# Optimization experiments

Measured on AMD Instinct MI355X. Metric: run time of the kernel, lower is better.

Reference implementation:

```python
import jax, jax.numpy as jnp
import numpy as np

N, K, D, E = 30000, 20, 128, 600000


def time_encode(t, w, b):
    # TGN TimeEncode: cos(Linear(1->D)(t)) ; t: [...], returns [..., D]
    return jnp.cos(t[..., None] * w + b)


def setup_inputs() -> dict:
    key = jax.random.key(0)
    ks = jax.random.split(key, 8)
    node_features = jax.random.normal(ks[0], (N, D), dtype=jnp.float32)
    timestamps = jax.random.uniform(ks[1], (N,), dtype=jnp.float32) * 1e4
    edge_features = jax.random.normal(ks[2], (E, D), dtype=jnp.float32)
    neighbors = jax.random.randint(ks[3], (N, K), 0, N, dtype=jnp.int32)
    edge_idxs = jax.random.randint(ks[4], (N, K), 0, E, dtype=jnp.int32)
    # edge interaction times precede the query timestamps (temporal neighbor sampling)
    edge_times = jax.random.uniform(ks[5], (N, K), dtype=jnp.float32) * timestamps[:, None]
    # TGN basis-frequency init for the time encoder
    time_w = (1.0 / 10.0 ** np.linspace(0, 9, D)).astype(np.float32)
    time_w = jnp.asarray(time_w)
    time_b = jnp.zeros((D,), dtype=jnp.float32)
    s1 = 1.0 / np.sqrt(3 * D)
    W1 = jax.random.normal(ks[6], (3 * D, D), dtype=jnp.float32) * s1
    b1 = jnp.zeros((D,), dtype=jnp.float32)
    W2 = jax.random.normal(ks[7], (3 * D, D), dtype=jnp.float32) * s1
    b2 = jnp.zeros((D,), dtype=jnp.float32)
    return {"node_features": node_features, "timestamps": timestamps,
            "edge_features": edge_features, "neighbors": neighbors,
            "edge_idxs": edge_idxs, "edge_times": edge_times,
            "time_w": time_w, "time_b": time_b,
            "W1": W1, "b1": b1, "W2": W2, "b2": b2}


def reference(node_features, timestamps, edge_features, neighbors, edge_idxs,
              edge_times, time_w, time_b, W1, b1, W2, b2):
    # layer-0 neighbor embeddings = raw node features gathered at neighbor ids
    neigh_feat = node_features[neighbors]                       # [N, K, D]
    # time deltas between query time and edge times, then cosine time encoding
    deltas = timestamps[:, None] - edge_times                   # [N, K]
    edge_time_emb = time_encode(deltas, time_w, time_b)         # [N, K, D]
    edge_feat = edge_features[edge_idxs]                        # [N, K, D]
    # GraphSumEmbedding.aggregate
    neighbors_features = jnp.concatenate(
        [neigh_feat, edge_time_emb, edge_feat], axis=-1)        # [N, K, 3D]
    h = neighbors_features @ W1 + b1                            # [N, K, D]
    neighbors_sum = jax.nn.relu(jnp.sum(h, axis=1))             # [N, D]
    src_time_emb = time_encode(jnp.zeros_like(timestamps), time_w, time_b)  # [N, D]
    source_features = jnp.concatenate([node_features, src_time_emb], axis=1)
    source_embedding = jnp.concatenate([neighbors_sum, source_features], axis=1)
    return source_embedding @ W2 + b2                           # [N, D]
```

## Files before the change

### kernel.cpp

```cpp
#include <hip/hip_runtime.h>
#include <math.h>

#define DD 128
#define KNB 20
#define K3 384
#define NPB 8

typedef unsigned short u16;
typedef __attribute__((ext_vector_type(8))) short short8;
typedef __attribute__((ext_vector_type(4))) float f32x4;

static __device__ __forceinline__ u16 f2bf(float x) {
    union { float f; unsigned u; } v; v.f = x;
    unsigned r = v.u + 0x7fffu + ((v.u >> 16) & 1u);
    return (u16)(r >> 16);
}

static __device__ __forceinline__ float fcos(float x) {
    float r = x * 0.15915494309189535f;
    r = __builtin_amdgcn_fractf(r);
    return __builtin_amdgcn_cosf(r);
}

static __device__ __forceinline__ void st4bf(u16* p, float4 v) {
    ushort4 s;
    s.x = f2bf(v.x); s.y = f2bf(v.y); s.z = f2bf(v.z); s.w = f2bf(v.w);
    *(ushort4*)p = s;
}

__global__ __launch_bounds__(DD) void const_kernel(
    const float* __restrict__ tb, const float* __restrict__ W2,
    const float* __restrict__ b2, float* __restrict__ cvec)
{
    int d = threadIdx.x;
    float acc = b2[d];
    #pragma unroll 8
    for (int i = 0; i < DD; ++i)
        acc = fmaf(cosf(tb[i]), W2[(size_t)(2 * DD + i) * DD + d], acc);
    cvec[d] = acc;
}

__global__ __launch_bounds__(256) void pack_w(
    const float* __restrict__ W1, const float* __restrict__ W2,
    u16* __restrict__ W1p, u16* __restrict__ W2p)
{
    int t = blockIdx.x * 256 + threadIdx.x;
    if (t < 6144) {
        int L = t & 63;
        int ct = (t >> 6) & 7;
        int kt = t >> 9;
        int n  = ct * 16 + (L & 15);
        int kb = kt * 32 + (L >> 4) * 8;
        u16* d = W1p + (size_t)t * 8;
        #pragma unroll
        for (int j = 0; j < 8; ++j) d[j] = f2bf(W1[(size_t)(kb + j) * DD + n]);
    } else if (t < 10240) {
        int u = t - 6144;
        int L = u & 63;
        int ct = (u >> 6) & 7;
        int kt = (u >> 9) & 3;
        int part = u >> 11;
        int n  = ct * 16 + (L & 15);
        int kb = part * DD + kt * 32 + (L >> 4) * 8;
        u16* d = W2p + (size_t)u * 8;
        #pragma unroll
        for (int j = 0; j < 8; ++j) d[j] = f2bf(W2[(size_t)(kb + j) * DD + n]);
    }
}

__global__ __launch_bounds__(256) void agg_kernel(
    const float* __restrict__ nodef, const float* __restrict__ ts,
    const float* __restrict__ edgef, const int* __restrict__ neighbors,
    const int* __restrict__ edge_idxs, const float* __restrict__ edge_times,
    const float* __restrict__ tw, const float* __restrict__ tb,
    u16* __restrict__ aggbf, u16* __restrict__ nfbf, int N)
{
    __shared__ int   s_nb[NPB * KNB];
    __shared__ int   s_eg[NPB * KNB];
    __shared__ float s_dt[NPB * KNB];

    const int tid = threadIdx.x;
    const int n0  = blockIdx.x * NPB;

    if (tid < NPB * KNB) {
        int nsub = tid / KNB;
        int k    = tid - nsub * KNB;
        int nn   = n0 + nsub;
        if (nn < N) {
            s_nb[tid] = neighbors[(size_t)nn * KNB + k];
            s_eg[tid] = edge_idxs[(size_t)nn * KNB + k];
            s_dt[tid] = ts[nn] - edge_times[(size_t)nn * KNB + k];
        } else {
            s_nb[tid] = 0; s_eg[tid] = 0; s_dt[tid] = 0.f;
        }
    }
    __syncthreads();

    const int c    = tid & 31;
    const int nsub = tid >> 5;
    const int n    = n0 + nsub;

    const float4* nf4 = (const float4*)nodef;
    const float4* ef4 = (const float4*)edgef;
    const float4  w4  = ((const float4*)tw)[c];
    const float4  b4  = ((const float4*)tb)[c];

    float4 an = make_float4(0.f, 0.f, 0.f, 0.f);
    float4 ae = an, at = an;

    const int*   nb  = s_nb + nsub * KNB;
    const int*   eg  = s_eg + nsub * KNB;
    const float* dtp = s_dt + nsub * KNB;

    #pragma unroll 10
    for (int k = 0; k < KNB; ++k) {
        int   ni = nb[k];
        int   ei = eg[k];
        float dt = dtp[k];
        float4 nv = nf4[(size_t)ni * 32 + c];
        float4 ev = ef4[(size_t)ei * 32 + c];
        an.x += nv.x; an.y += nv.y; an.z += nv.z; an.w += nv.w;
        ae.x += ev.x; ae.y += ev.y; ae.z += ev.z; ae.w += ev.w;
        at.x += fcos(fmaf(dt, w4.x, b4.x));
        at.y += fcos(fmaf(dt, w4.y, b4.y));
        at.z += fcos(fmaf(dt, w4.z, b4.z));
        at.w += fcos(fmaf(dt, w4.w, b4.w));
    }

    if (n < N) {
        u16* o = aggbf + (size_t)n * K3;
        st4bf(o + 4 * c,           an);
        st4bf(o + DD + 4 * c,      at);
        st4bf(o + 2 * DD + 4 * c,  ae);
        float4 sf = nf4[(size_t)n * 32 + c];
        st4bf(nfbf + (size_t)n * DD + 4 * c, sf);
    }
}

#define APITCH 392
#define HPITCH 136

__global__ __launch_bounds__(256) void fused_gemm(
    const u16* __restrict__ aggbf, const u16* __restrict__ nfbf,
    const u16* __restrict__ W1p, const u16* __restrict__ W2p,
    const float* __restrict__ b1, const float* __restrict__ cvec,
    float* __restrict__ out, int N)
{
    __shared__ __align__(16) u16 As[32 * APITCH];

    const int tid  = threadIdx.x;
    const int lane = tid & 63;
    const int wave = tid >> 6;
    const int row0 = blockIdx.x * 32;
    const int m0     = (wave & 1) * 16;
    const int ctbase = (wave >> 1) * 4;
    const int l15  = lane & 15;
    const int quad = lane >> 4;

    {
        const float4* ag4 = (const float4*)aggbf;
        #pragma unroll
        for (int i = 0; i < 6; ++i) {
            int idx = tid + i * 256;
            int r = idx / 48, c = idx - r * 48;
            float4 v = make_float4(0.f, 0.f, 0.f, 0.f);
            int row = row0 + r;
            if (row < N) v = ag4[(size_t)row * 48 + c];
            *(float4*)&As[r * APITCH + c * 8] = v;
        }
    }
    __syncthreads();

    f32x4 acc[4];
    #pragma unroll
    for (int c = 0; c < 4; ++c) acc[c] = (f32x4){0.f, 0.f, 0.f, 0.f};

    const short8* W1v = (const short8*)W1p;
    for (int kt = 0; kt < 12; ++kt) {
        short8 a = *(const short8*)&As[(m0 + l15) * APITCH + kt * 32 + quad * 8];
        #pragma unroll
        for (int c = 0; c < 4; ++c) {
            short8 b = W1v[(size_t)(kt * 8 + ctbase + c) * 64 + lane];
            acc[c] = __builtin_amdgcn_mfma_f32_16x16x32_bf16(a, b, acc[c], 0, 0, 0);
        }
    }
    __syncthreads();

    u16* Hs  = As;
    u16* NFs = As + 32 * HPITCH;
    #pragma unroll
    for (int c = 0; c < 4; ++c) {
        int col = (ctbase + c) * 16 + l15;
        float bb = (float)KNB * b1[col];
        #pragma unroll
        for (int r = 0; r < 4; ++r) {
            float h = acc[c][r] + bb;
            h = h > 0.f ? h : 0.f;
            Hs[(m0 + quad * 4 + r) * HPITCH + col] = f2bf(h);
        }
    }
    {
        const float4* nf4 = (const float4*)nfbf;
        #pragma unroll
        for (int i = 0; i < 2; ++i) {
            int idx = tid + i * 256;
            int r = idx >> 4, c = idx & 15;
            float4 v = make_float4(0.f, 0.f, 0.f, 0.f);
            int row = row0 + r;
            if (row < N) v = nf4[(size_t)row * 16 + c];
            *(float4*)&NFs[r * HPITCH + c * 8] = v;
        }
    }
    __syncthreads();

    f32x4 acc2[4];
    #pragma unroll
    for (int c = 0; c < 4; ++c) {
        float cv = cvec[(ctbase + c) * 16 + l15];
        acc2[c] = (f32x4){cv, cv, cv, cv};
    }
    const short8* W2v = (const short8*)W2p;
    for (int kt = 0; kt < 4; ++kt) {
        short8 aH = *(const short8*)&Hs[(m0 + l15) * HPITCH + kt * 32 + quad * 8];
        #pragma unroll
        for (int c = 0; c < 4; ++c) {
            short8 b = W2v[(size_t)(kt * 8 + ctbase + c) * 64 + lane];
            acc2[c] = __builtin_amdgcn_mfma_f32_16x16x32_bf16(aH, b, acc2[c], 0, 0, 0);
        }
        short8 aN = *(const short8*)&NFs[(m0 + l15) * HPITCH + kt * 32 + quad * 8];
        #pragma unroll
        for (int c = 0; c < 4; ++c) {
            short8 b = W2v[(size_t)((4 + kt) * 8 + ctbase + c) * 64 + lane];
            acc2[c] = __builtin_amdgcn_mfma_f32_16x16x32_bf16(aN, b, acc2[c], 0, 0, 0);
        }
    }

    #pragma unroll
    for (int c = 0; c < 4; ++c) {
        int col = (ctbase + c) * 16 + l15;
        #pragma unroll
        for (int r = 0; r < 4; ++r) {
            int row = row0 + m0 + quad * 4 + r;
            if (row < N) out[(size_t)row * DD + col] = acc2[c][r];
        }
    }
}

extern "C" void kernel_launch(void* const* d_in, const int* in_sizes, int n_in,
                              void* d_out, int out_size, void* d_ws, size_t ws_size,
                              hipStream_t stream)
{
    const float* nodef      = (const float*)d_in[0];
    const float* ts         = (const float*)d_in[1];
    const float* edgef      = (const float*)d_in[2];
    const int*   neighbors  = (const int*)d_in[3];
    const int*   edge_idxs  = (const int*)d_in[4];
    const float* edge_times = (const float*)d_in[5];
    const float* tw         = (const float*)d_in[6];
    const float* tb         = (const float*)d_in[7];
    const float* W1         = (const float*)d_in[8];
    const float* b1         = (const float*)d_in[9];
    const float* W2         = (const float*)d_in[10];
    const float* b2         = (const float*)d_in[11];
    float*       out        = (float*)d_out;

    const int N = in_sizes[1];

    u16*   aggbf = (u16*)d_ws;
    u16*   nfbf  = aggbf + (size_t)N * K3;
    u16*   W1p   = nfbf + (size_t)N * DD;
    u16*   W2p   = W1p + 12 * 8 * 64 * 8;
    float* cvec  = (float*)(W2p + 2 * 4 * 8 * 64 * 8);

    hipLaunchKernelGGL(const_kernel, dim3(1), dim3(DD), 0, stream,
                       tb, W2, b2, cvec);
    hipLaunchKernelGGL(pack_w, dim3(40), dim3(256), 0, stream,
                       W1, W2, W1p, W2p);
    hipLaunchKernelGGL(agg_kernel, dim3((N + NPB - 1) / NPB), dim3(256), 0, stream,
                       nodef, ts, edgef, neighbors, edge_idxs, edge_times,
                       tw, tb, aggbf, nfbf, N);
    hipLaunchKernelGGL(fused_gemm, dim3((N + 31) / 32), dim3(256), 0, stream,
                       aggbf, nfbf, W1p, W2p, b1, cvec, out, N);
}
```

Before: 481.2 us.

## Fuse neighbor aggregation with both GEMMs and merge the prep kernels

Merges the aggregation kernel and the two-stage MFMA GEMM into one kernel that keeps the aggregated bf16 rows and node features in LDS. This removes the global round trip through the aggbf/nfbf workspace. Each block now handles 16 rows, with each thread-group gathering two rows, and the four waves split the output columns. The weight-packing and constant-vector kernels are also combined into a single launch. The trade-off is a smaller M tile per block, so each block reloads the weight fragments over fewer rows.

```diff
diff --git a/kernel.cpp b/kernel.cpp
--- a/kernel.cpp
+++ b/kernel.cpp
@@ -4,7 +4,7 @@
 #define DD 128
 #define KNB 20
 #define K3 384
-#define NPB 8
+#define ROWS 16
 
 typedef unsigned short u16;
 typedef __attribute__((ext_vector_type(8))) short short8;
@@ -28,220 +28,211 @@
     *(ushort4*)p = s;
 }
 
-__global__ __launch_bounds__(DD) void const_kernel(
-    const float* __restrict__ tb, const float* __restrict__ W2,
-    const float* __restrict__ b2, float* __restrict__ cvec)
+__global__ __launch_bounds__(256) void prep_kernel(
+    const float* __restrict__ W1, const float* __restrict__ W2,
+    const float* __restrict__ tb, const float* __restrict__ b2,
+    u16* __restrict__ W1p, u16* __restrict__ W2p, float* __restrict__ cvec)
 {
-    int d = threadIdx.x;
-    float acc = b2[d];
-    #pragma unroll 8
-    for (int i = 0; i < DD; ++i)
-        acc = fmaf(cosf(tb[i]), W2[(size_t)(2 * DD + i) * DD + d], acc);
-    cvec[d] = acc;
-}
-
-__global__ __launch_bounds__(256) void pack_w(
-    const float* __restrict__ W1, const float* __restrict__ W2,
-    u16* __restrict__ W1p, u16* __restrict__ W2p)
-{
-    int t = blockIdx.x * 256 + threadIdx.x;
-    if (t < 6144) {
-        int L = t & 63;
-        int ct = (t >> 6) & 7;
-        int kt = t >> 9;
-        int n  = ct * 16 + (L & 15);
-        int kb = kt * 32 + (L >> 4) * 8;
-        u16* d = W1p + (size_t)t * 8;
-        #pragma unroll
-        for (int j = 0; j < 8; ++j) d[j] = f2bf(W1[(size_t)(kb + j) * DD + n]);
-    } else if (t < 10240) {
-        int u = t - 6144;
-        int L = u & 63;
-        int ct = (u >> 6) & 7;
-        int kt = (u >> 9) & 3;
-        int part = u >> 11;
-        int n  = ct * 16 + (L & 15);
-        int kb = part * DD + kt * 32 + (L >> 4) * 8;
-        u16* d = W2p + (size_t)u * 8;
-        #pragma unroll
-        for (int j = 0; j < 8; ++j) d[j] = f2bf(W2[(size_t)(kb + j) * DD + n]);
-    }
-}
-
-__global__ __launch_bounds__(256) void agg_kernel(
+    const int tid = threadIdx.x;
+    if (blockIdx.x < 40) {
+        int t = blockIdx.x * 256 + tid;
+        if (t < 6144) {
+            int L = t & 63;
+            int ct = (t >> 6) & 7;
+            int kt = t >> 9;
+            int n  = ct * 16 + (L & 15);
+            int kb = kt * 32 + (L >> 4) * 8;
+            u16* d = W1p + (size_t)t * 8;
+            #pragma unroll
+            for (int j = 0; j < 8; ++j) d[j] = f2bf(W1[(size_t)(kb + j) * DD + n]);
+        } else if (t < 10240) {
+            int u = t - 6144;
+            int L = u & 63;
+            int ct = (u >> 6) & 7;
+            int kt = (u >> 9) & 3;
+            int part = u >> 11;
+            int n  = ct * 16 + (L & 15);
+            int kb = part * DD + kt * 32 + (L >> 4) * 8;
+            u16* d = W2p + (size_t)u * 8;
+            #pragma unroll
+            for (int j = 0; j < 8; ++j) d[j] = f2bf(W2[(size_t)(kb + j) * DD + n]);
+        }
+    } else {
+        __shared__ float red[DD];
+        int d = tid & (DD - 1);
+        int h = tid >> 7;
+        float acc = 0.f;
+        int i0 = h * 64;
+        #pragma unroll 8
+        for (int i = i0; i < i0 + 64; ++i)
+            acc = fmaf(cosf(tb[i]), W2[(size_t)(2 * DD + i) * DD + d], acc);
+        if (h) red[d] = acc;
+        __syncthreads();
+        if (!h) cvec[d] = acc + red[d] + b2[d];
+    }
+}
+
+#define APITCH 392
+#define HPITCH 136
+
+__global__ __launch_bounds__(256, 4) void fused_all(
     const float* __restrict__ nodef, const float* __restrict__ ts,
     const float* __restrict__ edgef, const int* __restrict__ neighbors,
     const int* __restrict__ edge_idxs, const float* __restrict__ edge_times,
     const float* __restrict__ tw, const float* __restrict__ tb,
-    u16* __restrict__ aggbf, u16* __restrict__ nfbf, int N)
-{
-    __shared__ int   s_nb[NPB * KNB];
-    __shared__ int   s_eg[NPB * KNB];
-    __shared__ float s_dt[NPB * KNB];
-
-    const int tid = threadIdx.x;
-    const int n0  = blockIdx.x * NPB;
-
-    if (tid < NPB * KNB) {
-        int nsub = tid / KNB;
-        int k    = tid - nsub * KNB;
-        int nn   = n0 + nsub;
-        if (nn < N) {
-            s_nb[tid] = neighbors[(size_t)nn * KNB + k];
-            s_eg[tid] = edge_idxs[(size_t)nn * KNB + k];
-            s_dt[tid] = ts[nn] - edge_times[(size_t)nn * KNB + k];
-        } else {
-            s_nb[tid] = 0; s_eg[tid] = 0; s_dt[tid] = 0.f;
-        }
-    }
-    __syncthreads();
-
-    const int c    = tid & 31;
-    const int nsub = tid >> 5;
-    const int n    = n0 + nsub;
-
-    const float4* nf4 = (const float4*)nodef;
-    const float4* ef4 = (const float4*)edgef;
-    const float4  w4  = ((const float4*)tw)[c];
-    const float4  b4  = ((const float4*)tb)[c];
-
-    float4 an = make_float4(0.f, 0.f, 0.f, 0.f);
-    float4 ae = an, at = an;
-
-    const int*   nb  = s_nb + nsub * KNB;
-    const int*   eg  = s_eg + nsub * KNB;
-    const float* dtp = s_dt + nsub * KNB;
-
-    #pragma unroll 10
-    for (int k = 0; k < KNB; ++k) {
-        int   ni = nb[k];
-        int   ei = eg[k];
-        float dt = dtp[k];
-        float4 nv = nf4[(size_t)ni * 32 + c];
-        float4 ev = ef4[(size_t)ei * 32 + c];
-        an.x += nv.x; an.y += nv.y; an.z += nv.z; an.w += nv.w;
-        ae.x += ev.x; ae.y += ev.y; ae.z += ev.z; ae.w += ev.w;
-        at.x += fcos(fmaf(dt, w4.x, b4.x));
-        at.y += fcos(fmaf(dt, w4.y, b4.y));
-        at.z += fcos(fmaf(dt, w4.z, b4.z));
-        at.w += fcos(fmaf(dt, w4.w, b4.w));
-    }
-
-    if (n < N) {
-        u16* o = aggbf + (size_t)n * K3;
-        st4bf(o + 4 * c,           an);
-        st4bf(o + DD + 4 * c,      at);
-        st4bf(o + 2 * DD + 4 * c,  ae);
-        float4 sf = nf4[(size_t)n * 32 + c];
-        st4bf(nfbf + (size_t)n * DD + 4 * c, sf);
-    }
-}
-
-#define APITCH 392
-#define HPITCH 136
-
-__global__ __launch_bounds__(256) void fused_gemm(
-    const u16* __restrict__ aggbf, const u16* __restrict__ nfbf,
     const u16* __restrict__ W1p, const u16* __restrict__ W2p,
     const float* __restrict__ b1, const float* __restrict__ cvec,
     float* __restrict__ out, int N)
 {
-    __shared__ __align__(16) u16 As[32 * APITCH];
+    __shared__ __align__(16) u16 As[ROWS * APITCH];
+    __shared__ __align__(16) u16 NFs[ROWS * HPITCH];
+    __shared__ int   s_nb[ROWS * KNB];
+    __shared__ int   s_eg[ROWS * KNB];
+    __shared__ float s_dt[ROWS * KNB];
 
     const int tid  = threadIdx.x;
+    const int row0 = blockIdx.x * ROWS;
+
+    for (int idx = tid; idx < ROWS * KNB; idx += 256) {
+        int nsub = idx / KNB;
+        int k    = idx - nsub * KNB;
+        int nn   = row0 + nsub;
+        if (nn < N) {
+            s_nb[idx] = neighbors[(size_t)nn * KNB + k];
+            s_eg[idx] = edge_idxs[(size_t)nn * KNB + k];
+            s_dt[idx] = ts[nn] - edge_times[(size_t)nn * KNB + k];
+        } else {
+            s_nb[idx] = 0; s_eg[idx] = 0; s_dt[idx] = 0.f;
+        }
+    }
+    __syncthreads();
+
+    {
+        const int c  = tid & 31;
+        const int g  = tid >> 5;
+        const int ra = g, rb = g + 8;
+
+        const float4* nf4 = (const float4*)nodef;
+        const float4* ef4 = (const float4*)edgef;
+        const float4  w4  = ((const float4*)tw)[c];
+        const float4  b4  = ((const float4*)tb)[c];
+
+        const int*   nba = s_nb + ra * KNB;
+        const int*   ega = s_eg + ra * KNB;
+        const float* dpa = s_dt + ra * KNB;
+        const int*   nbb = s_nb + rb * KNB;
+        const int*   egb = s_eg + rb * KNB;
+        const float* dpb = s_dt + rb * KNB;
+
+        float4 z = make_float4(0.f, 0.f, 0.f, 0.f);
+        float4 ana = z, aea = z, ata = z;
+        float4 anb = z, aeb = z, atb = z;
+
+        #pragma unroll 4
+        for (int k = 0; k < KNB; ++k) {
+            int   nia = nba[k], eia = ega[k];
+            int   nib = nbb[k], eib = egb[k];
+            float dta = dpa[k], dtb = dpb[k];
+            float4 nva = nf4[(size_t)nia * 32 + c];
+            float4 eva = ef4[(size_t)eia * 32 + c];
+            float4 nvb = nf4[(size_t)nib * 32 + c];
+            float4 evb = ef4[(size_t)eib * 32 + c];
+            ana.x += nva.x; ana.y += nva.y; ana.z += nva.z; ana.w += nva.w;
+            aea.x += eva.x; aea.y += eva.y; aea.z += eva.z; aea.w += eva.w;
+            anb.x += nvb.x; anb.y += nvb.y; anb.z += nvb.z; anb.w += nvb.w;
+            aeb.x += evb.x; aeb.y += evb.y; aeb.z += evb.z; aeb.w += evb.w;
+            ata.x += fcos(fmaf(dta, w4.x, b4.x));
+            ata.y += fcos(fmaf(dta, w4.y, b4.y));
+            ata.z += fcos(fmaf(dta, w4.z, b4.z));
+            ata.w += fcos(fmaf(dta, w4.w, b4.w));
+            atb.x += fcos(fmaf(dtb, w4.x, b4.x));
+            atb.y += fcos(fmaf(dtb, w4.y, b4.y));
+            atb.z += fcos(fmaf(dtb, w4.z, b4.z));
+            atb.w += fcos(fmaf(dtb, w4.w, b4.w));
+        }
+
+        u16* oa = As + ra * APITCH;
+        st4bf(oa + 4 * c,          ana);
+        st4bf(oa + DD + 4 * c,     ata);
+        st4bf(oa + 2 * DD + 4 * c, aea);
+        u16* ob = As + rb * APITCH;
+        st4bf(ob + 4 * c,          anb);
+        st4bf(ob + DD + 4 * c,     atb);
+        st4bf(ob + 2 * DD + 4 * c, aeb);
+
+        int na = row0 + ra;
+        float4 sa = (na < N) ? nf4[(size_t)na * 32 + c] : z;
+        st4bf(NFs + ra * HPITCH + 4 * c, sa);
+        int nb_ = row0 + rb;
+        float4 sb = (nb_ < N) ? nf4[(size_t)nb_ * 32 + c] : z;
+        st4bf(NFs + rb * HPITCH + 4 * c, sb);
+    }
+    __syncthreads();
+
     const int lane = tid & 63;
     const int wave = tid >> 6;
-    const int row0 = blockIdx.x * 32;
-    const int m0     = (wave & 1) * 16;
-    const int ctbase = (wave >> 1) * 4;
     const int l15  = lane & 15;
     const int quad = lane >> 4;
-
-    {
-        const float4* ag4 = (const float4*)aggbf;
-        #pragma unroll
-        for (int i = 0; i < 6; ++i) {
-            int idx = tid + i * 256;
-            int r = idx / 48, c = idx - r * 48;
-            float4 v = make_float4(0.f, 0.f, 0.f, 0.f);
-            int row = row0 + r;
-            if (row < N) v = ag4[(size_t)row * 48 + c];
-            *(float4*)&As[r * APITCH + c * 8] = v;
-        }
-    }
-    __syncthreads();
-
-    f32x4 acc[4];
-    #pragma unroll
-    for (int c = 0; c < 4; ++c) acc[c] = (f32x4){0.f, 0.f, 0.f, 0.f};
+    const int ct0  = wave * 2;
+
+    f32x4 acc[2];
+    acc[0] = (f32x4){0.f, 0.f, 0.f, 0.f};
+    acc[1] = (f32x4){0.f, 0.f, 0.f, 0.f};
 
     const short8* W1v = (const short8*)W1p;
     for (int kt = 0; kt < 12; ++kt) {
-        short8 a = *(const short8*)&As[(m0 + l15) * APITCH + kt * 32 + quad * 8];
-        #pragma unroll
-        for (int c = 0; c < 4; ++c) {
-            short8 b = W1v[(size_t)(kt * 8 + ctbase + c) * 64 + lane];
-            acc[c] = __builtin_amdgcn_mfma_f32_16x16x32_bf16(a, b, acc[c], 0, 0, 0);
-        }
-    }
-    __syncthreads();
-
-    u16* Hs  = As;
-    u16* NFs = As + 32 * HPITCH;
+        short8 a = *(const short8*)&As[l15 * APITCH + kt * 32 + quad * 8];
+        #pragma unroll
+        for (int cc = 0; cc < 2; ++cc) {
+            short8 b = W1v[(size_t)(kt * 8 + ct0 + cc) * 64 + lane];
+            acc[cc] = __builtin_amdgcn_mfma_f32_16x16x32_bf16(a, b, acc[cc], 0, 0, 0);
+        }
+    }
+    __syncthreads();
+
+    u16* Hs = As;
     #pragma unroll
-    for (int c = 0; c < 4; ++c) {
-        int col = (ctbase + c) * 16 + l15;
+    for (int cc = 0; cc < 2; ++cc) {
+        int col = (ct0 + cc) * 16 + l15;
         float bb = (float)KNB * b1[col];
         #pragma unroll
         for (int r = 0; r < 4; ++r) {
-            float h = acc[c][r] + bb;
+            float h = acc[cc][r] + bb;
             h = h > 0.f ? h : 0.f;
-            Hs[(m0 + quad * 4 + r) * HPITCH + col] = f2bf(h);
-        }
-    }
-    {
-        const float4* nf4 = (const float4*)nfbf;
-        #pragma unroll
-        for (int i = 0; i < 2; ++i) {
-            int idx = tid + i * 256;
-            int r = idx >> 4, c = idx & 15;
-            float4 v = make_float4(0.f, 0.f, 0.f, 0.f);
-            int row = row0 + r;
-            if (row < N) v = nf4[(size_t)row * 16 + c];
-            *(float4*)&NFs[r * HPITCH + c * 8] = v;
-        }
-    }
-    __syncthreads();
-
-    f32x4 acc2[4];
+            Hs[(quad * 4 + r) * HPITCH + col] = f2bf(h);
+        }
+    }
+    __syncthreads();
+
+    f32x4 acc2[2];
     #pragma unroll
-    for (int c = 0; c < 4; ++c) {
-        float cv = cvec[(ctbase + c) * 16 + l15];
-        acc2[c] = (f32x4){cv, cv, cv, cv};
+    for (int cc = 0; cc < 2; ++cc) {
+        float cv = cvec[(ct0 + cc) * 16 + l15];
+        acc2[cc] = (f32x4){cv, cv, cv, cv};
     }
     const short8* W2v = (const short8*)W2p;
     for (int kt = 0; kt < 4; ++kt) {
-        short8 aH = *(const short8*)&Hs[(m0 + l15) * HPITCH + kt * 32 + quad * 8];
-        #pragma unroll
-        for (int c = 0; c < 4; ++c) {
-            short8 b = W2v[(size_t)(kt * 8 + ctbase + c) * 64 + lane];
-            acc2[c] = __builtin_amdgcn_mfma_f32_16x16x32_bf16(aH, b, acc2[c], 0, 0, 0);
-        }
-        short8 aN = *(const short8*)&NFs[(m0 + l15) * HPITCH + kt * 32 + quad * 8];
-        #pragma unroll
-        for (int c = 0; c < 4; ++c) {
-            short8 b = W2v[(size_t)((4 + kt) * 8 + ctbase + c) * 64 + lane];
-            acc2[c] = __builtin_amdgcn_mfma_f32_16x16x32_bf16(aN, b, acc2[c], 0, 0, 0);
+        short8 aH = *(const short8*)&Hs[l15 * HPITCH + kt * 32 + quad * 8];
+        #pragma unroll
+        for (int cc = 0; cc < 2; ++cc) {
+            short8 b = W2v[(size_t)(kt * 8 + ct0 + cc) * 64 + lane];
+            acc2[cc] = __builtin_amdgcn_mfma_f32_16x16x32_bf16(aH, b, acc2[cc], 0, 0, 0);
+        }
+        short8 aN = *(const short8*)&NFs[l15 * HPITCH + kt * 32 + quad * 8];
+        #pragma unroll
+        for (int cc = 0; cc < 2; ++cc) {
+            short8 b = W2v[(size_t)((4 + kt) * 8 + ct0 + cc) * 64 + lane];
+            acc2[cc] = __builtin_amdgcn_mfma_f32_16x16x32_bf16(aN, b, acc2[cc], 0, 0, 0);
         }
     }
 
     #pragma unroll
-    for (int c = 0; c < 4; ++c) {
-        int col = (ctbase + c) * 16 + l15;
+    for (int cc = 0; cc < 2; ++cc) {
+        int col = (ct0 + cc) * 16 + l15;
         #pragma unroll
         for (int r = 0; r < 4; ++r) {
-            int row = row0 + m0 + quad * 4 + r;
-            if (row < N) out[(size_t)row * DD + col] = acc2[c][r];
+            int row = row0 + quad * 4 + r;
+            if (row < N) out[(size_t)row * DD + col] = acc2[cc][r];
         }
     }
 }
@@ -266,19 +257,13 @@
 
     const int N = in_sizes[1];
 
-    u16*   aggbf = (u16*)d_ws;
-    u16*   nfbf  = aggbf + (size_t)N * K3;
-    u16*   W1p   = nfbf + (size_t)N * DD;
-    u16*   W2p   = W1p + 12 * 8 * 64 * 8;
-    float* cvec  = (float*)(W2p + 2 * 4 * 8 * 64 * 8);
-
-    hipLaunchKernelGGL(const_kernel, dim3(1), dim3(DD), 0, stream,
-                       tb, W2, b2, cvec);
-    hipLaunchKernelGGL(pack_w, dim3(40), dim3(256), 0, stream,
-                       W1, W2, W1p, W2p);
-    hipLaunchKernelGGL(agg_kernel, dim3((N + NPB - 1) / NPB), dim3(256), 0, stream,
+    u16*   W1p  = (u16*)d_ws;
+    u16*   W2p  = W1p + 12 * 8 * 64 * 8;
+    float* cvec = (float*)(W2p + 2 * 4 * 8 * 64 * 8);
+
+    hipLaunchKernelGGL(prep_kernel, dim3(41), dim3(256), 0, stream,
+                       W1, W2, tb, b2, W1p, W2p, cvec);
+    hipLaunchKernelGGL(fused_all, dim3((N + ROWS - 1) / ROWS), dim3(256), 0, stream,
                        nodef, ts, edgef, neighbors, edge_idxs, edge_times,
-                       tw, tb, aggbf, nfbf, N);
-    hipLaunchKernelGGL(fused_gemm, dim3((N + 31) / 32), dim3(256), 0, stream,
-                       aggbf, nfbf, W1p, W2p, b1, cvec, out, N);
-}
+                       tw, tb, W1p, W2p, b1, cvec, out, N);
+}
```

New measurement: 472.9 us. About the same (-1.7%).
